# Performance work log

Hardware: AMD Instinct MI355X
Metric: run time of the kernel (lower is better)

## Reference

```python
import jax, jax.numpy as jnp
import numpy as np

M = 100000      # number of simplices
NNZ = 800000    # nonzeros per Laplacian (avg degree 8)
B = 2
C_IN = 64
C_OUT = 64
K1 = 3
K2 = 3


def setup_inputs() -> dict:
    key = jax.random.key(0)
    ks = jax.random.split(key, 7)
    Ll_indices = jax.random.randint(ks[0], (2, NNZ), 0, M, dtype=jnp.int32)
    Ll_values = jax.random.normal(ks[1], (NNZ,), dtype=jnp.float32) * 0.1
    Lu_indices = jax.random.randint(ks[2], (2, NNZ), 0, M, dtype=jnp.int32)
    Lu_values = jax.random.normal(ks[3], (NNZ,), dtype=jnp.float32) * 0.1
    x = jax.random.normal(ks[4], (B, C_IN, M), dtype=jnp.float32)
    theta = jax.random.normal(ks[5], (C_OUT, C_IN, K1 + K2), dtype=jnp.float32)
    bias = jnp.zeros((1, C_OUT, 1), dtype=jnp.float32)
    return {"Ll_indices": Ll_indices, "Ll_values": Ll_values,
            "Lu_indices": Lu_indices, "Lu_values": Lu_values,
            "x": x, "theta": theta, "bias": bias}


def _spmm(rows, cols, vals, x):
    # sparse (M,M) @ x along last axis; x: (B, C, M) -> (B, C, M)
    gathered = x[:, :, cols] * vals            # (B, C, nnz)
    return jnp.zeros_like(x).at[:, :, rows].add(gathered)


def _assemble_powers(K, rows, cols, vals, x):
    outs = [x]
    for _ in range(K - 1):
        outs.append(_spmm(rows, cols, vals, outs[-1]))
    return jnp.stack(outs, axis=3)             # (B, C, M, K)


def reference(Ll_indices, Ll_values, Lu_indices, Lu_values, x, theta, bias):
    X1 = _assemble_powers(K1, Ll_indices[0], Ll_indices[1], Ll_values, x)
    X2 = _assemble_powers(K2, Lu_indices[0], Lu_indices[1], Lu_values, x)
    X = jnp.concatenate((X1, X2), axis=3)      # (B, C_in, M, K1+K2)
    y = jnp.einsum('bimk,oik->bom', X, theta)  # (B, C_out, M)
    return y + bias
```

## Files before the change

kernel.cpp:

```cpp
#include <hip/hip_runtime.h>
#include <stdint.h>

#define M_SIMP 100000
#define MPAD   100064
#define NNZV   800000
#define KM5    5

typedef unsigned int u32;
typedef __attribute__((ext_vector_type(8))) short short8;
typedef __attribute__((ext_vector_type(4))) float f32x4;

__device__ __forceinline__ float bf2f(u32 u){ return __uint_as_float(u << 16); }
__device__ __forceinline__ u32 f2bf(float f){
    u32 u = __float_as_uint(f);
    return (u + 0x7FFFu + ((u >> 16) & 1u)) >> 16;
}

__global__ void k_histpe(const int* __restrict__ i0, int* __restrict__ c0, int* __restrict__ p0,
                         const int* __restrict__ i1, int* __restrict__ c1, int* __restrict__ p1){
    int e = blockIdx.x * 256 + threadIdx.x;
    const int* idx = blockIdx.y ? i1 : i0;
    int* cnt = blockIdx.y ? c1 : c0;
    int* pe  = blockIdx.y ? p1 : p0;
    if (e < NNZV){
        int r = idx[e];
        pe[e] = atomicAdd(&cnt[r], 1);
    }
}

__global__ void k_scan1(const int* __restrict__ in0, int* __restrict__ out0, int* __restrict__ bs0,
                        const int* __restrict__ in1, int* __restrict__ out1, int* __restrict__ bs1,
                        int n){
    const int* in  = blockIdx.y ? in1 : in0;
    int* out   = blockIdx.y ? out1 : out0;
    int* bsums = blockIdx.y ? bs1 : bs0;
    __shared__ int s[256];
    int t = threadIdx.x;
    int base = blockIdx.x * 1024 + t * 4;
    int v0 = (base + 0 < n) ? in[base + 0] : 0;
    int v1 = (base + 1 < n) ? in[base + 1] : 0;
    int v2 = (base + 2 < n) ? in[base + 2] : 0;
    int v3 = (base + 3 < n) ? in[base + 3] : 0;
    int sum = v0 + v1 + v2 + v3;
    s[t] = sum;
    __syncthreads();
    for (int off = 1; off < 256; off <<= 1){
        int x = (t >= off) ? s[t - off] : 0;
        __syncthreads();
        s[t] += x;
        __syncthreads();
    }
    int excl = s[t] - sum;
    if (t == 255) bsums[blockIdx.x] = s[255];
    if (base + 0 < n) out[base + 0] = excl;
    if (base + 1 < n) out[base + 1] = excl + v0;
    if (base + 2 < n) out[base + 2] = excl + v0 + v1;
    if (base + 3 < n) out[base + 3] = excl + v0 + v1 + v2;
}

__global__ void k_scan2(int* __restrict__ b0, int* __restrict__ b1,
                        int* __restrict__ rp0, int* __restrict__ rp1, int nb){
    int t = threadIdx.x;
    if (t < 2){
        int* bs = t ? b1 : b0;
        int run = 0;
        for (int i = 0; i < nb; i++){ int x = bs[i]; bs[i] = run; run += x; }
    }
    if (t == 2) rp0[M_SIMP] = NNZV;
    if (t == 3) rp1[M_SIMP] = NNZV;
}

__global__ void k_scan3(int* __restrict__ o0, const int* __restrict__ b0,
                        int* __restrict__ o1, const int* __restrict__ b1, int n){
    int* out = blockIdx.y ? o1 : o0;
    const int* bsums = blockIdx.y ? b1 : b0;
    int base = blockIdx.x * 1024 + threadIdx.x * 4;
    int add = bsums[blockIdx.x];
    #pragma unroll
    for (int j = 0; j < 4; j++)
        if (base + j < n) out[base + j] += add;
}

__global__ void k_scatcv(const int* __restrict__ i0, const float* __restrict__ v0,
                         const int* __restrict__ pe0, const int* __restrict__ rp0,
                         uint2* __restrict__ cv0,
                         const int* __restrict__ i1, const float* __restrict__ v1,
                         const int* __restrict__ pe1, const int* __restrict__ rp1,
                         uint2* __restrict__ cv1){
    int e = blockIdx.x * 256 + threadIdx.x;
    const int* idx   = blockIdx.y ? i1 : i0;
    const float* val = blockIdx.y ? v1 : v0;
    const int* pe    = blockIdx.y ? pe1 : pe0;
    const int* rp    = blockIdx.y ? rp1 : rp0;
    uint2* cv        = blockIdx.y ? cv1 : cv0;
    if (e < NNZV){
        int r = idx[e];
        uint2 o;
        o.x = (u32)idx[NNZV + e];
        o.y = __float_as_uint(val[e]);
        cv[rp[r] + pe[e]] = o;
    }
}

__global__ void k_transpose(const float* __restrict__ x, u32* __restrict__ F0){
    __shared__ unsigned short s[64 * 130];
    int t = threadIdx.x;
    int m0 = blockIdx.x * 64;
    int j  = t & 63;
    int r4 = t >> 6;
    #pragma unroll 4
    for (int it = 0; it < 32; ++it){
        int bc = it * 4 + r4;
        int m  = m0 + j;
        if (m < M_SIMP)
            s[j * 130 + bc] = (unsigned short)f2bf(x[(size_t)bc * M_SIMP + m]);
    }
    __syncthreads();
    #pragma unroll 4
    for (int it = 0; it < 16; ++it){
        int m  = it * 4 + r4;
        int gm = m0 + m;
        if (gm < M_SIMP){
            u32 lo = s[m * 130 + 2 * j];
            u32 hi = s[m * 130 + 2 * j + 1];
            F0[(size_t)gm * 64 + j] = lo | (hi << 16);
        }
    }
}

__global__ __launch_bounds__(256) void k_spmm(
    const int* __restrict__ rpA, const uint2* __restrict__ cvA,
    const u32* __restrict__ finA, u32* __restrict__ foutA,
    const int* __restrict__ rpB, const uint2* __restrict__ cvB,
    const u32* __restrict__ finB, u32* __restrict__ foutB)
{
    int t   = threadIdx.x;
    int sub = t >> 4;
    int l   = t & 15;
    int row = blockIdx.x * 16 + sub;
    const int* rp; const uint2* cv; const u32* fin; u32* fout;
    if (blockIdx.y == 0){ rp=rpA; cv=cvA; fin=finA; fout=foutA; }
    else                { rp=rpB; cv=cvB; fin=finB; fout=foutB; }
    if (row >= M_SIMP) return;
    int s = rp[row], en = rp[row + 1];
    float a0=0,a1=0,a2=0,a3=0,a4=0,a5=0,a6=0,a7=0;
    int j = s;
    for (; j + 4 <= en; j += 4){
        uint2 q0 = cv[j], q1 = cv[j+1], q2 = cv[j+2], q3 = cv[j+3];
        uint4 g0 = *(const uint4*)(fin + (size_t)q0.x * 64 + l * 4);
        uint4 g1 = *(const uint4*)(fin + (size_t)q1.x * 64 + l * 4);
        uint4 g2 = *(const uint4*)(fin + (size_t)q2.x * 64 + l * 4);
        uint4 g3 = *(const uint4*)(fin + (size_t)q3.x * 64 + l * 4);
        float v0 = __uint_as_float(q0.y), v1 = __uint_as_float(q1.y);
        float v2 = __uint_as_float(q2.y), v3 = __uint_as_float(q3.y);
        a0 += v0*bf2f(g0.x&0xffffu) + v1*bf2f(g1.x&0xffffu) + v2*bf2f(g2.x&0xffffu) + v3*bf2f(g3.x&0xffffu);
        a1 += v0*bf2f(g0.x>>16)     + v1*bf2f(g1.x>>16)     + v2*bf2f(g2.x>>16)     + v3*bf2f(g3.x>>16);
        a2 += v0*bf2f(g0.y&0xffffu) + v1*bf2f(g1.y&0xffffu) + v2*bf2f(g2.y&0xffffu) + v3*bf2f(g3.y&0xffffu);
        a3 += v0*bf2f(g0.y>>16)     + v1*bf2f(g1.y>>16)     + v2*bf2f(g2.y>>16)     + v3*bf2f(g3.y>>16);
        a4 += v0*bf2f(g0.z&0xffffu) + v1*bf2f(g1.z&0xffffu) + v2*bf2f(g2.z&0xffffu) + v3*bf2f(g3.z&0xffffu);
        a5 += v0*bf2f(g0.z>>16)     + v1*bf2f(g1.z>>16)     + v2*bf2f(g2.z>>16)     + v3*bf2f(g3.z>>16);
        a6 += v0*bf2f(g0.w&0xffffu) + v1*bf2f(g1.w&0xffffu) + v2*bf2f(g2.w&0xffffu) + v3*bf2f(g3.w&0xffffu);
        a7 += v0*bf2f(g0.w>>16)     + v1*bf2f(g1.w>>16)     + v2*bf2f(g2.w>>16)     + v3*bf2f(g3.w>>16);
    }
    for (; j < en; j++){
        uint2 q = cv[j];
        float v = __uint_as_float(q.y);
        uint4 g = *(const uint4*)(fin + (size_t)q.x * 64 + l * 4);
        a0 += v*bf2f(g.x&0xffffu); a1 += v*bf2f(g.x>>16);
        a2 += v*bf2f(g.y&0xffffu); a3 += v*bf2f(g.y>>16);
        a4 += v*bf2f(g.z&0xffffu); a5 += v*bf2f(g.z>>16);
        a6 += v*bf2f(g.w&0xffffu); a7 += v*bf2f(g.w>>16);
    }
    uint4 o;
    o.x = f2bf(a0) | (f2bf(a1) << 16);
    o.y = f2bf(a2) | (f2bf(a3) << 16);
    o.z = f2bf(a4) | (f2bf(a5) << 16);
    o.w = f2bf(a6) | (f2bf(a7) << 16);
    *(uint4*)(fout + (size_t)row * 64 + l * 4) = o;
}

__global__ void k_wb(const float* __restrict__ theta, u32* __restrict__ Wb){
    int idx = blockIdx.x * 256 + threadIdx.x;
    if (idx < KM5 * 64 * 32){
        int km = idx >> 11;
        int r  = idx & 2047;
        int o  = r >> 5;
        int i2 = (r & 31) * 2;
        int k  = (km == 0) ? 0 : ((km < 3) ? km : km + 1);
        float lo = theta[o * 384 + i2 * 6 + k];
        float hi = theta[o * 384 + (i2 + 1) * 6 + k];
        if (km == 0){
            lo += theta[o * 384 + i2 * 6 + 3];
            hi += theta[o * 384 + (i2 + 1) * 6 + 3];
        }
        Wb[idx] = f2bf(lo) | (f2bf(hi) << 16);
    }
}

__global__ __launch_bounds__(256, 4) void k_gemm(
    const u32* __restrict__ F0, const u32* __restrict__ F1, const u32* __restrict__ F2,
    const u32* __restrict__ F4, const u32* __restrict__ F5,
    const u32* __restrict__ Wb, const float* __restrict__ bias, float* __restrict__ out)
{
    __shared__ __align__(16) u32 sh[2][4096];
    int t    = threadIdx.x;
    int wave = t >> 6;
    int lane = t & 63;
    int q    = lane >> 4;
    int l16  = lane & 15;
    int bm   = blockIdx.x * 64;
    const u32* __restrict__ Fs[KM5] = {F0, F1, F2, F4, F5};

    int rowbase  = t >> 4;
    int srcc     = (t & 15) ^ ((t >> 4) & 15);
    int wavebase = (t & 192) * 4;

    f32x4 a00 = {0.f,0.f,0.f,0.f}, a10 = {0.f,0.f,0.f,0.f};
    f32x4 a20 = {0.f,0.f,0.f,0.f}, a30 = {0.f,0.f,0.f,0.f};
    f32x4 a01 = {0.f,0.f,0.f,0.f}, a11 = {0.f,0.f,0.f,0.f};
    f32x4 a21 = {0.f,0.f,0.f,0.f}, a31 = {0.f,0.f,0.f,0.f};

    int o_a = wave * 16 + l16;

    short8 wc0 = *(const short8*)(Wb + (0 * 64 + o_a) * 32 + 0 * 16 + q * 4);
    short8 wc1 = *(const short8*)(Wb + (0 * 64 + o_a) * 32 + 1 * 16 + q * 4);

    #pragma unroll
    for (int i = 0; i < 4; ++i){
        const u32* g = Fs[0] + (size_t)(bm + i * 16 + rowbase) * 64 + srcc * 4;
        __builtin_amdgcn_global_load_lds(g, &sh[0][i * 1024 + wavebase], 16, 0, 0);
    }
    asm volatile("s_waitcnt vmcnt(0)" ::: "memory");
    __syncthreads();

    #pragma unroll
    for (int km = 0; km < KM5; ++km){
        short8 wn0 = wc0, wn1 = wc1;
        if (km < KM5 - 1){
            wn0 = *(const short8*)(Wb + ((km + 1) * 64 + o_a) * 32 + 0 * 16 + q * 4);
            wn1 = *(const short8*)(Wb + ((km + 1) * 64 + o_a) * 32 + 1 * 16 + q * 4);
            const u32* __restrict__ Fn = Fs[km + 1];
            u32* dst = &sh[(km + 1) & 1][0];
            #pragma unroll
            for (int i = 0; i < 4; ++i){
                const u32* g = Fn + (size_t)(bm + i * 16 + rowbase) * 64 + srcc * 4;
                __builtin_amdgcn_global_load_lds(g, dst + i * 1024 + wavebase, 16, 0, 0);
            }
        }

        const u32* Lb = &sh[km & 1][0];
        #pragma unroll
        for (int h = 0; h < 2; ++h){
            short8 wa = h ? wc1 : wc0;
            int c0 = ((h * 4 + q) ^ l16) * 4;
            int c1 = ((8 + h * 4 + q) ^ l16) * 4;
            #pragma unroll
            for (int ms = 0; ms < 4; ++ms){
                const u32* rp_ = Lb + ms * 1024 + l16 * 64;
                short8 b0 = *(const short8*)(rp_ + c0);
                short8 b1 = *(const short8*)(rp_ + c1);
                if (ms == 0){ a00 = __builtin_amdgcn_mfma_f32_16x16x32_bf16(wa, b0, a00, 0, 0, 0);
                              a01 = __builtin_amdgcn_mfma_f32_16x16x32_bf16(wa, b1, a01, 0, 0, 0); }
                if (ms == 1){ a10 = __builtin_amdgcn_mfma_f32_16x16x32_bf16(wa, b0, a10, 0, 0, 0);
                              a11 = __builtin_amdgcn_mfma_f32_16x16x32_bf16(wa, b1, a11, 0, 0, 0); }
                if (ms == 2){ a20 = __builtin_amdgcn_mfma_f32_16x16x32_bf16(wa, b0, a20, 0, 0, 0);
                              a21 = __builtin_amdgcn_mfma_f32_16x16x32_bf16(wa, b1, a21, 0, 0, 0); }
                if (ms == 3){ a30 = __builtin_amdgcn_mfma_f32_16x16x32_bf16(wa, b0, a30, 0, 0, 0);
                              a31 = __builtin_amdgcn_mfma_f32_16x16x32_bf16(wa, b1, a31, 0, 0, 0); }
            }
        }

        asm volatile("s_waitcnt vmcnt(0)" ::: "memory");
        __syncthreads();
        wc0 = wn0; wc1 = wn1;
    }

    int ob = wave * 16 + q * 4;
    float bv0 = bias[ob], bv1 = bias[ob+1], bv2 = bias[ob+2], bv3 = bias[ob+3];
    f32x4 accs0[4] = {a00, a10, a20, a30};
    f32x4 accs1[4] = {a01, a11, a21, a31};
    #pragma unroll
    for (int ms = 0; ms < 4; ms++){
        int gm = bm + ms * 16 + l16;
        if (gm < M_SIMP){
            size_t base0 = (size_t)(0 * 64 + ob) * M_SIMP + gm;
            size_t base1 = (size_t)(1 * 64 + ob) * M_SIMP + gm;
            out[base0             ] = accs0[ms][0] + bv0;
            out[base0 + 1ul*M_SIMP] = accs0[ms][1] + bv1;
            out[base0 + 2ul*M_SIMP] = accs0[ms][2] + bv2;
            out[base0 + 3ul*M_SIMP] = accs0[ms][3] + bv3;
            out[base1             ] = accs1[ms][0] + bv0;
            out[base1 + 1ul*M_SIMP] = accs1[ms][1] + bv1;
            out[base1 + 2ul*M_SIMP] = accs1[ms][2] + bv2;
            out[base1 + 3ul*M_SIMP] = accs1[ms][3] + bv3;
        }
    }
}

extern "C" void kernel_launch(void* const* d_in, const int* in_sizes, int n_in,
                              void* d_out, int out_size, void* d_ws, size_t ws_size,
                              hipStream_t stream)
{
    const int*   Ll_idx = (const int*)d_in[0];
    const float* Ll_val = (const float*)d_in[1];
    const int*   Lu_idx = (const int*)d_in[2];
    const float* Lu_val = (const float*)d_in[3];
    const float* x      = (const float*)d_in[4];
    const float* theta  = (const float*)d_in[5];
    const float* bias   = (const float*)d_in[6];
    float* out = (float*)d_out;

    char* ws = (char*)d_ws;
    size_t off = 0;
    auto take = [&](size_t bytes) -> char* {
        char* p = ws + off;
        off = (off + bytes + 255) & ~(size_t)255;
        return p;
    };
    const size_t FB = (size_t)MPAD * 64 * 4;
    u32* F0 = (u32*)take(FB);
    u32* F1 = (u32*)take(FB);
    u32* F2 = (u32*)take(FB);
    u32* F4 = (u32*)take(FB);
    u32* F5 = (u32*)take(FB);
    u32* Wb = (u32*)take((size_t)KM5 * 64 * 32 * 4);
    int* cnt_l = (int*)take((size_t)M_SIMP * 4);
    int* cnt_u = (int*)take((size_t)M_SIMP * 4);
    int* rp_l  = (int*)take((size_t)(M_SIMP + 1) * 4);
    int* rp_u  = (int*)take((size_t)(M_SIMP + 1) * 4);
    int* pe_l  = (int*)take((size_t)NNZV * 4);
    int* pe_u  = (int*)take((size_t)NNZV * 4);
    uint2* cv_l = (uint2*)take((size_t)NNZV * 8);
    uint2* cv_u = (uint2*)take((size_t)NNZV * 8);
    int* bs_l = (int*)take(512);
    int* bs_u = (int*)take(512);

    hipMemsetAsync(cnt_l, 0, (size_t)M_SIMP * 4, stream);
    hipMemsetAsync(cnt_u, 0, (size_t)M_SIMP * 4, stream);

    const int NBH = (NNZV + 255) / 256;
    dim3 gh(NBH, 2);
    k_histpe<<<gh, 256, 0, stream>>>(Ll_idx, cnt_l, pe_l, Lu_idx, cnt_u, pe_u);

    const int NBS = (M_SIMP + 1023) / 1024;
    dim3 gs(NBS, 2);
    k_scan1<<<gs, 256, 0, stream>>>(cnt_l, rp_l, bs_l, cnt_u, rp_u, bs_u, M_SIMP);
    k_scan2<<<1, 64, 0, stream>>>(bs_l, bs_u, rp_l, rp_u, NBS);
    k_scan3<<<gs, 256, 0, stream>>>(rp_l, bs_l, rp_u, bs_u, M_SIMP);

    k_scatcv<<<gh, 256, 0, stream>>>(Ll_idx, Ll_val, pe_l, rp_l, cv_l,
                                     Lu_idx, Lu_val, pe_u, rp_u, cv_u);

    const int NBT = (M_SIMP + 63) / 64;
    k_transpose<<<NBT, 256, 0, stream>>>(x, F0);
    k_wb<<<(KM5 * 64 * 32 + 255) / 256, 256, 0, stream>>>(theta, Wb);

    const int NBM = (M_SIMP + 15) / 16;
    dim3 gm(NBM, 2);
    k_spmm<<<gm, 256, 0, stream>>>(rp_l, cv_l, F0, F1,
                                   rp_u, cv_u, F0, F4);
    k_spmm<<<gm, 256, 0, stream>>>(rp_l, cv_l, F1, F2,
                                   rp_u, cv_u, F4, F5);

    k_gemm<<<NBT, 256, 0, stream>>>(F0, F1, F2, F4, F5, Wb, bias, out);
}
```

Measured before the change: 411.2 us.

## Privatize CSR row histogram per XCC and fuse front-end kernels

Row counting for CSR construction now uses eight per-XCC counter arrays selected by the hardware XCC id, with workgroup-scope relaxed atomics, so atomics avoid cross-die coherence traffic. The scan kernels are extended to turn the eight counter copies into per-XCC row offsets, which the scatter uses. The histogram, transpose/bf16 conversion and weight packing are merged into one launch to cut launch overhead. In exchange it adds an 8x larger memset and extra scan traffic, and it relies on workgroup-scope atomics staying correct across CUs that share an XCC.

Measured after the change: 403.3 us. About the same (-1.9%).

```diff
diff --git a/kernel.cpp b/kernel.cpp
--- a/kernel.cpp
+++ b/kernel.cpp
@@ -5,6 +5,9 @@
 #define MPAD   100064
 #define NNZV   800000
 #define KM5    5
+#define NBH    3125
+#define NBT    1563
+#define NBW    40
 
 typedef unsigned int u32;
 typedef __attribute__((ext_vector_type(8))) short short8;
@@ -16,32 +19,93 @@
     return (u + 0x7FFFu + ((u >> 16) & 1u)) >> 16;
 }
 
-__global__ void k_histpe(const int* __restrict__ i0, int* __restrict__ c0, int* __restrict__ p0,
-                         const int* __restrict__ i1, int* __restrict__ c1, int* __restrict__ p1){
-    int e = blockIdx.x * 256 + threadIdx.x;
-    const int* idx = blockIdx.y ? i1 : i0;
-    int* cnt = blockIdx.y ? c1 : c0;
-    int* pe  = blockIdx.y ? p1 : p0;
-    if (e < NNZV){
-        int r = idx[e];
-        pe[e] = atomicAdd(&cnt[r], 1);
-    }
-}
-
-__global__ void k_scan1(const int* __restrict__ in0, int* __restrict__ out0, int* __restrict__ bs0,
-                        const int* __restrict__ in1, int* __restrict__ out1, int* __restrict__ bs1,
+__global__ void k_front(const int* __restrict__ Ll_idx, const int* __restrict__ Lu_idx,
+                        int* __restrict__ cnt8_l, int* __restrict__ cnt8_u,
+                        u32* __restrict__ pe_l, u32* __restrict__ pe_u,
+                        const float* __restrict__ x, u32* __restrict__ F0,
+                        const float* __restrict__ theta, u32* __restrict__ Wb)
+{
+    __shared__ unsigned short s[64 * 130];
+    int bid = blockIdx.x;
+    int t   = threadIdx.x;
+
+    if (bid < 2 * NBH){
+        int lap = (bid >= NBH);
+        const int* idx = lap ? Lu_idx : Ll_idx;
+        int* cnt8      = lap ? cnt8_u : cnt8_l;
+        u32* pe        = lap ? pe_u  : pe_l;
+        int e = (bid - lap * NBH) * 256 + t;
+        u32 xcc;
+        asm volatile("s_getreg_b32 %0, hwreg(HW_REG_XCC_ID)" : "=s"(xcc));
+        xcc &= 7u;
+        if (e < NNZV){
+            int r = idx[e];
+            u32 p = __hip_atomic_fetch_add((u32*)&cnt8[xcc * M_SIMP + r], 1u,
+                                           __ATOMIC_RELAXED, __HIP_MEMORY_SCOPE_WORKGROUP);
+            pe[e] = p | (xcc << 24);
+        }
+    } else if (bid < 2 * NBH + NBT){
+        int m0 = (bid - 2 * NBH) * 64;
+        int j  = t & 63;
+        int r4 = t >> 6;
+        #pragma unroll 4
+        for (int it = 0; it < 32; ++it){
+            int bc = it * 4 + r4;
+            int m  = m0 + j;
+            if (m < M_SIMP)
+                s[j * 130 + bc] = (unsigned short)f2bf(x[(size_t)bc * M_SIMP + m]);
+        }
+        __syncthreads();
+        #pragma unroll 4
+        for (int it = 0; it < 16; ++it){
+            int m  = it * 4 + r4;
+            int gm = m0 + m;
+            if (gm < M_SIMP){
+                u32 lo = s[m * 130 + 2 * j];
+                u32 hi = s[m * 130 + 2 * j + 1];
+                F0[(size_t)gm * 64 + j] = lo | (hi << 16);
+            }
+        }
+    } else {
+        int idx = (bid - 2 * NBH - NBT) * 256 + t;
+        if (idx < KM5 * 64 * 32){
+            int km = idx >> 11;
+            int r  = idx & 2047;
+            int o  = r >> 5;
+            int i2 = (r & 31) * 2;
+            int k  = (km == 0) ? 0 : ((km < 3) ? km : km + 1);
+            float lo = theta[o * 384 + i2 * 6 + k];
+            float hi = theta[o * 384 + (i2 + 1) * 6 + k];
+            if (km == 0){
+                lo += theta[o * 384 + i2 * 6 + 3];
+                hi += theta[o * 384 + (i2 + 1) * 6 + 3];
+            }
+            Wb[idx] = f2bf(lo) | (f2bf(hi) << 16);
+        }
+    }
+}
+
+__global__ void k_scan1(int* __restrict__ cnt0, int* __restrict__ out0, int* __restrict__ bs0,
+                        int* __restrict__ cnt1, int* __restrict__ out1, int* __restrict__ bs1,
                         int n){
-    const int* in  = blockIdx.y ? in1 : in0;
+    int* cnt   = blockIdx.y ? cnt1 : cnt0;
     int* out   = blockIdx.y ? out1 : out0;
     int* bsums = blockIdx.y ? bs1 : bs0;
     __shared__ int s[256];
     int t = threadIdx.x;
     int base = blockIdx.x * 1024 + t * 4;
-    int v0 = (base + 0 < n) ? in[base + 0] : 0;
-    int v1 = (base + 1 < n) ? in[base + 1] : 0;
-    int v2 = (base + 2 < n) ? in[base + 2] : 0;
-    int v3 = (base + 3 < n) ? in[base + 3] : 0;
-    int sum = v0 + v1 + v2 + v3;
+    int c[8][4];
+    int tot[4] = {0,0,0,0};
+    bool ok = (base < n);
+    if (ok){
+        #pragma unroll
+        for (int i = 0; i < 8; i++){
+            int4 v = *(const int4*)(cnt + (size_t)i * M_SIMP + base);
+            c[i][0]=v.x; c[i][1]=v.y; c[i][2]=v.z; c[i][3]=v.w;
+            tot[0]+=v.x; tot[1]+=v.y; tot[2]+=v.z; tot[3]+=v.w;
+        }
+    }
+    int sum = tot[0]+tot[1]+tot[2]+tot[3];
     s[t] = sum;
     __syncthreads();
     for (int off = 1; off < 256; off <<= 1){
@@ -52,10 +116,20 @@
     }
     int excl = s[t] - sum;
     if (t == 255) bsums[blockIdx.x] = s[255];
-    if (base + 0 < n) out[base + 0] = excl;
-    if (base + 1 < n) out[base + 1] = excl + v0;
-    if (base + 2 < n) out[base + 2] = excl + v0 + v1;
-    if (base + 3 < n) out[base + 3] = excl + v0 + v1 + v2;
+    if (ok){
+        int ro[4];
+        ro[0] = excl;
+        ro[1] = ro[0] + tot[0];
+        ro[2] = ro[1] + tot[1];
+        ro[3] = ro[2] + tot[2];
+        *(int4*)(out + base) = make_int4(ro[0], ro[1], ro[2], ro[3]);
+        int p0=ro[0], p1=ro[1], p2=ro[2], p3=ro[3];
+        #pragma unroll
+        for (int i = 0; i < 8; i++){
+            *(int4*)(cnt + (size_t)i * M_SIMP + base) = make_int4(p0, p1, p2, p3);
+            p0 += c[i][0]; p1 += c[i][1]; p2 += c[i][2]; p3 += c[i][3];
+        }
+    }
 }
 
 __global__ void k_scan2(int* __restrict__ b0, int* __restrict__ b1,
@@ -70,61 +144,45 @@
     if (t == 3) rp1[M_SIMP] = NNZV;
 }
 
-__global__ void k_scan3(int* __restrict__ o0, const int* __restrict__ b0,
-                        int* __restrict__ o1, const int* __restrict__ b1, int n){
+__global__ void k_scan3(int* __restrict__ o0, const int* __restrict__ b0, int* __restrict__ c0,
+                        int* __restrict__ o1, const int* __restrict__ b1, int* __restrict__ c1,
+                        int n){
     int* out = blockIdx.y ? o1 : o0;
     const int* bsums = blockIdx.y ? b1 : b0;
+    int* c8  = blockIdx.y ? c1 : c0;
     int base = blockIdx.x * 1024 + threadIdx.x * 4;
     int add = bsums[blockIdx.x];
-    #pragma unroll
-    for (int j = 0; j < 4; j++)
-        if (base + j < n) out[base + j] += add;
+    if (base < n){
+        int4* po = (int4*)(out + base);
+        int4 v = *po; v.x+=add; v.y+=add; v.z+=add; v.w+=add; *po = v;
+        #pragma unroll
+        for (int i = 0; i < 8; i++){
+            int4* pc = (int4*)(c8 + (size_t)i * M_SIMP + base);
+            int4 u = *pc; u.x+=add; u.y+=add; u.z+=add; u.w+=add; *pc = u;
+        }
+    }
 }
 
 __global__ void k_scatcv(const int* __restrict__ i0, const float* __restrict__ v0,
-                         const int* __restrict__ pe0, const int* __restrict__ rp0,
+                         const u32* __restrict__ pe0, const int* __restrict__ c8_0,
                          uint2* __restrict__ cv0,
                          const int* __restrict__ i1, const float* __restrict__ v1,
-                         const int* __restrict__ pe1, const int* __restrict__ rp1,
+                         const u32* __restrict__ pe1, const int* __restrict__ c8_1,
                          uint2* __restrict__ cv1){
     int e = blockIdx.x * 256 + threadIdx.x;
     const int* idx   = blockIdx.y ? i1 : i0;
     const float* val = blockIdx.y ? v1 : v0;
-    const int* pe    = blockIdx.y ? pe1 : pe0;
-    const int* rp    = blockIdx.y ? rp1 : rp0;
+    const u32* pe    = blockIdx.y ? pe1 : pe0;
+    const int* c8    = blockIdx.y ? c8_1 : c8_0;
     uint2* cv        = blockIdx.y ? cv1 : cv0;
     if (e < NNZV){
         int r = idx[e];
+        u32 pr = pe[e];
+        int pos = c8[(size_t)(pr >> 24) * M_SIMP + r] + (int)(pr & 0xFFFFFFu);
         uint2 o;
         o.x = (u32)idx[NNZV + e];
         o.y = __float_as_uint(val[e]);
-        cv[rp[r] + pe[e]] = o;
-    }
-}
-
-__global__ void k_transpose(const float* __restrict__ x, u32* __restrict__ F0){
-    __shared__ unsigned short s[64 * 130];
-    int t = threadIdx.x;
-    int m0 = blockIdx.x * 64;
-    int j  = t & 63;
-    int r4 = t >> 6;
-    #pragma unroll 4
-    for (int it = 0; it < 32; ++it){
-        int bc = it * 4 + r4;
-        int m  = m0 + j;
-        if (m < M_SIMP)
-            s[j * 130 + bc] = (unsigned short)f2bf(x[(size_t)bc * M_SIMP + m]);
-    }
-    __syncthreads();
-    #pragma unroll 4
-    for (int it = 0; it < 16; ++it){
-        int m  = it * 4 + r4;
-        int gm = m0 + m;
-        if (gm < M_SIMP){
-            u32 lo = s[m * 130 + 2 * j];
-            u32 hi = s[m * 130 + 2 * j + 1];
-            F0[(size_t)gm * 64 + j] = lo | (hi << 16);
-        }
+        cv[pos] = o;
     }
 }
 
@@ -179,24 +237,6 @@
     *(uint4*)(fout + (size_t)row * 64 + l * 4) = o;
 }
 
-__global__ void k_wb(const float* __restrict__ theta, u32* __restrict__ Wb){
-    int idx = blockIdx.x * 256 + threadIdx.x;
-    if (idx < KM5 * 64 * 32){
-        int km = idx >> 11;
-        int r  = idx & 2047;
-        int o  = r >> 5;
-        int i2 = (r & 31) * 2;
-        int k  = (km == 0) ? 0 : ((km < 3) ? km : km + 1);
-        float lo = theta[o * 384 + i2 * 6 + k];
-        float hi = theta[o * 384 + (i2 + 1) * 6 + k];
-        if (km == 0){
-            lo += theta[o * 384 + i2 * 6 + 3];
-            hi += theta[o * 384 + (i2 + 1) * 6 + 3];
-        }
-        Wb[idx] = f2bf(lo) | (f2bf(hi) << 16);
-    }
-}
-
 __global__ __launch_bounds__(256, 4) void k_gemm(
     const u32* __restrict__ F0, const u32* __restrict__ F1, const u32* __restrict__ F2,
     const u32* __restrict__ F4, const u32* __restrict__ F5,
@@ -324,36 +364,32 @@
     u32* F4 = (u32*)take(FB);
     u32* F5 = (u32*)take(FB);
     u32* Wb = (u32*)take((size_t)KM5 * 64 * 32 * 4);
-    int* cnt_l = (int*)take((size_t)M_SIMP * 4);
-    int* cnt_u = (int*)take((size_t)M_SIMP * 4);
+    int* cnt8_l = (int*)take((size_t)8 * M_SIMP * 4);
+    int* cnt8_u = (int*)take((size_t)8 * M_SIMP * 4);
     int* rp_l  = (int*)take((size_t)(M_SIMP + 1) * 4);
     int* rp_u  = (int*)take((size_t)(M_SIMP + 1) * 4);
-    int* pe_l  = (int*)take((size_t)NNZV * 4);
-    int* pe_u  = (int*)take((size_t)NNZV * 4);
+    u32* pe_l  = (u32*)take((size_t)NNZV * 4);
+    u32* pe_u  = (u32*)take((size_t)NNZV * 4);
     uint2* cv_l = (uint2*)take((size_t)NNZV * 8);
     uint2* cv_u = (uint2*)take((size_t)NNZV * 8);
     int* bs_l = (int*)take(512);
     int* bs_u = (int*)take(512);
 
-    hipMemsetAsync(cnt_l, 0, (size_t)M_SIMP * 4, stream);
-    hipMemsetAsync(cnt_u, 0, (size_t)M_SIMP * 4, stream);
-
-    const int NBH = (NNZV + 255) / 256;
-    dim3 gh(NBH, 2);
-    k_histpe<<<gh, 256, 0, stream>>>(Ll_idx, cnt_l, pe_l, Lu_idx, cnt_u, pe_u);
+    hipMemsetAsync(cnt8_l, 0, (size_t)8 * M_SIMP * 4, stream);
+    hipMemsetAsync(cnt8_u, 0, (size_t)8 * M_SIMP * 4, stream);
+
+    k_front<<<2 * NBH + NBT + NBW, 256, 0, stream>>>(
+        Ll_idx, Lu_idx, cnt8_l, cnt8_u, pe_l, pe_u, x, F0, theta, Wb);
 
     const int NBS = (M_SIMP + 1023) / 1024;
     dim3 gs(NBS, 2);
-    k_scan1<<<gs, 256, 0, stream>>>(cnt_l, rp_l, bs_l, cnt_u, rp_u, bs_u, M_SIMP);
+    k_scan1<<<gs, 256, 0, stream>>>(cnt8_l, rp_l, bs_l, cnt8_u, rp_u, bs_u, M_SIMP);
     k_scan2<<<1, 64, 0, stream>>>(bs_l, bs_u, rp_l, rp_u, NBS);
-    k_scan3<<<gs, 256, 0, stream>>>(rp_l, bs_l, rp_u, bs_u, M_SIMP);
-
-    k_scatcv<<<gh, 256, 0, stream>>>(Ll_idx, Ll_val, pe_l, rp_l, cv_l,
-                                     Lu_idx, Lu_val, pe_u, rp_u, cv_u);
-
-    const int NBT = (M_SIMP + 63) / 64;
-    k_transpose<<<NBT, 256, 0, stream>>>(x, F0);
-    k_wb<<<(KM5 * 64 * 32 + 255) / 256, 256, 0, stream>>>(theta, Wb);
+    k_scan3<<<gs, 256, 0, stream>>>(rp_l, bs_l, cnt8_l, rp_u, bs_u, cnt8_u, M_SIMP);
+
+    dim3 gh(NBH, 2);
+    k_scatcv<<<gh, 256, 0, stream>>>(Ll_idx, Ll_val, pe_l, cnt8_l, cv_l,
+                                     Lu_idx, Lu_val, pe_u, cnt8_u, cv_u);
 
     const int NBM = (M_SIMP + 15) / 16;
     dim3 gm(NBM, 2);
```

## Interleave Ll/Lu CSR build stages with SpMM via role-dispatched fused kernels

Applied to the files above, without the earlier changes.

Replaces the separate histogram, scan, scatter, transpose and SpMM launches with fused kernels. Each block picks a role from its block index, so the Lu CSR build (hist, scan, scatter) runs alongside the Ll SpMM passes. The scan2 kernel is dropped: scan3 now reduces the block sums in shared memory itself. The intent is fewer launches and more overlap of independent small stages. The cost is extra divergence in role dispatch and more shared memory per block, which may lower occupancy for the SpMM blocks.

Result: faster. 389.4 us (-5.3%).

```diff
diff --git a/kernel.cpp b/kernel.cpp
--- a/kernel.cpp
+++ b/kernel.cpp
@@ -5,6 +5,11 @@
 #define MPAD   100064
 #define NNZV   800000
 #define KM5    5
+#define NBH    3125
+#define NBT    1563
+#define NBW    40
+#define NBM    6250
+#define NBS    98
 
 typedef unsigned int u32;
 typedef __attribute__((ext_vector_type(8))) short short8;
@@ -16,96 +21,20 @@
     return (u + 0x7FFFu + ((u >> 16) & 1u)) >> 16;
 }
 
-__global__ void k_histpe(const int* __restrict__ i0, int* __restrict__ c0, int* __restrict__ p0,
-                         const int* __restrict__ i1, int* __restrict__ c1, int* __restrict__ p1){
-    int e = blockIdx.x * 256 + threadIdx.x;
-    const int* idx = blockIdx.y ? i1 : i0;
-    int* cnt = blockIdx.y ? c1 : c0;
-    int* pe  = blockIdx.y ? p1 : p0;
+
+__device__ __forceinline__ void role_hist(int h, int t, const int* __restrict__ idx,
+                                          int* __restrict__ cnt, u32* __restrict__ pe){
+    int e = h * 256 + t;
     if (e < NNZV){
         int r = idx[e];
-        pe[e] = atomicAdd(&cnt[r], 1);
-    }
-}
-
-__global__ void k_scan1(const int* __restrict__ in0, int* __restrict__ out0, int* __restrict__ bs0,
-                        const int* __restrict__ in1, int* __restrict__ out1, int* __restrict__ bs1,
-                        int n){
-    const int* in  = blockIdx.y ? in1 : in0;
-    int* out   = blockIdx.y ? out1 : out0;
-    int* bsums = blockIdx.y ? bs1 : bs0;
-    __shared__ int s[256];
-    int t = threadIdx.x;
-    int base = blockIdx.x * 1024 + t * 4;
-    int v0 = (base + 0 < n) ? in[base + 0] : 0;
-    int v1 = (base + 1 < n) ? in[base + 1] : 0;
-    int v2 = (base + 2 < n) ? in[base + 2] : 0;
-    int v3 = (base + 3 < n) ? in[base + 3] : 0;
-    int sum = v0 + v1 + v2 + v3;
-    s[t] = sum;
-    __syncthreads();
-    for (int off = 1; off < 256; off <<= 1){
-        int x = (t >= off) ? s[t - off] : 0;
-        __syncthreads();
-        s[t] += x;
-        __syncthreads();
-    }
-    int excl = s[t] - sum;
-    if (t == 255) bsums[blockIdx.x] = s[255];
-    if (base + 0 < n) out[base + 0] = excl;
-    if (base + 1 < n) out[base + 1] = excl + v0;
-    if (base + 2 < n) out[base + 2] = excl + v0 + v1;
-    if (base + 3 < n) out[base + 3] = excl + v0 + v1 + v2;
-}
-
-__global__ void k_scan2(int* __restrict__ b0, int* __restrict__ b1,
-                        int* __restrict__ rp0, int* __restrict__ rp1, int nb){
-    int t = threadIdx.x;
-    if (t < 2){
-        int* bs = t ? b1 : b0;
-        int run = 0;
-        for (int i = 0; i < nb; i++){ int x = bs[i]; bs[i] = run; run += x; }
-    }
-    if (t == 2) rp0[M_SIMP] = NNZV;
-    if (t == 3) rp1[M_SIMP] = NNZV;
-}
-
-__global__ void k_scan3(int* __restrict__ o0, const int* __restrict__ b0,
-                        int* __restrict__ o1, const int* __restrict__ b1, int n){
-    int* out = blockIdx.y ? o1 : o0;
-    const int* bsums = blockIdx.y ? b1 : b0;
-    int base = blockIdx.x * 1024 + threadIdx.x * 4;
-    int add = bsums[blockIdx.x];
-    #pragma unroll
-    for (int j = 0; j < 4; j++)
-        if (base + j < n) out[base + j] += add;
-}
-
-__global__ void k_scatcv(const int* __restrict__ i0, const float* __restrict__ v0,
-                         const int* __restrict__ pe0, const int* __restrict__ rp0,
-                         uint2* __restrict__ cv0,
-                         const int* __restrict__ i1, const float* __restrict__ v1,
-                         const int* __restrict__ pe1, const int* __restrict__ rp1,
-                         uint2* __restrict__ cv1){
-    int e = blockIdx.x * 256 + threadIdx.x;
-    const int* idx   = blockIdx.y ? i1 : i0;
-    const float* val = blockIdx.y ? v1 : v0;
-    const int* pe    = blockIdx.y ? pe1 : pe0;
-    const int* rp    = blockIdx.y ? rp1 : rp0;
-    uint2* cv        = blockIdx.y ? cv1 : cv0;
-    if (e < NNZV){
-        int r = idx[e];
-        uint2 o;
-        o.x = (u32)idx[NNZV + e];
-        o.y = __float_as_uint(val[e]);
-        cv[rp[r] + pe[e]] = o;
-    }
-}
-
-__global__ void k_transpose(const float* __restrict__ x, u32* __restrict__ F0){
+        pe[e] = (u32)atomicAdd(&cnt[r], 1);
+    }
+}
+
+__device__ __forceinline__ void role_transpose(int g, int t, const float* __restrict__ x,
+                                               u32* __restrict__ F0){
     __shared__ unsigned short s[64 * 130];
-    int t = threadIdx.x;
-    int m0 = blockIdx.x * 64;
+    int m0 = g * 64;
     int j  = t & 63;
     int r4 = t >> 6;
     #pragma unroll 4
@@ -128,19 +57,92 @@
     }
 }
 
-__global__ __launch_bounds__(256) void k_spmm(
-    const int* __restrict__ rpA, const uint2* __restrict__ cvA,
-    const u32* __restrict__ finA, u32* __restrict__ foutA,
-    const int* __restrict__ rpB, const uint2* __restrict__ cvB,
-    const u32* __restrict__ finB, u32* __restrict__ foutB)
-{
-    int t   = threadIdx.x;
+__device__ __forceinline__ void role_wb(int g, int t, const float* __restrict__ theta,
+                                        u32* __restrict__ Wb){
+    int idx = g * 256 + t;
+    if (idx < KM5 * 64 * 32){
+        int km = idx >> 11;
+        int r  = idx & 2047;
+        int o  = r >> 5;
+        int i2 = (r & 31) * 2;
+        int k  = (km == 0) ? 0 : ((km < 3) ? km : km + 1);
+        float lo = theta[o * 384 + i2 * 6 + k];
+        float hi = theta[o * 384 + (i2 + 1) * 6 + k];
+        if (km == 0){
+            lo += theta[o * 384 + i2 * 6 + 3];
+            hi += theta[o * 384 + (i2 + 1) * 6 + 3];
+        }
+        Wb[idx] = f2bf(lo) | (f2bf(hi) << 16);
+    }
+}
+
+__device__ __forceinline__ void role_scan1(int b, int t, const int* __restrict__ in,
+                                           int* __restrict__ out, int* __restrict__ bsums){
+    __shared__ int s1[256];
+    int base = b * 1024 + t * 4;
+    int v0 = (base + 0 < M_SIMP) ? in[base + 0] : 0;
+    int v1 = (base + 1 < M_SIMP) ? in[base + 1] : 0;
+    int v2 = (base + 2 < M_SIMP) ? in[base + 2] : 0;
+    int v3 = (base + 3 < M_SIMP) ? in[base + 3] : 0;
+    int sum = v0 + v1 + v2 + v3;
+    s1[t] = sum;
+    __syncthreads();
+    for (int off = 1; off < 256; off <<= 1){
+        int x = (t >= off) ? s1[t - off] : 0;
+        __syncthreads();
+        s1[t] += x;
+        __syncthreads();
+    }
+    int excl = s1[t] - sum;
+    if (t == 255) bsums[b] = s1[255];
+    if (base + 0 < M_SIMP) out[base + 0] = excl;
+    if (base + 1 < M_SIMP) out[base + 1] = excl + v0;
+    if (base + 2 < M_SIMP) out[base + 2] = excl + v0 + v1;
+    if (base + 3 < M_SIMP) out[base + 3] = excl + v0 + v1 + v2;
+}
+
+__device__ __forceinline__ void role_scan3(int b, int t, int* __restrict__ out,
+                                           const int* __restrict__ bsums){
+    __shared__ int sb[256];
+    sb[t] = (t < b && t < NBS) ? bsums[t] : 0;
+    __syncthreads();
+    #pragma unroll
+    for (int off = 128; off > 0; off >>= 1){
+        if (t < off) sb[t] += sb[t + off];
+        __syncthreads();
+    }
+    int add = sb[0];
+    if (t == 255 && b == 0) out[M_SIMP] = NNZV;
+    int base = b * 1024 + t * 4;
+    if (base < M_SIMP){
+        int4* po = (int4*)(out + base);
+        int4 v = *po; v.x += add; v.y += add; v.z += add; v.w += add; *po = v;
+    }
+}
+
+__device__ __forceinline__ void role_scatcv(int b, int t, const int* __restrict__ idx,
+                                            const float* __restrict__ val,
+                                            const u32* __restrict__ pe,
+                                            const int* __restrict__ rp,
+                                            uint2* __restrict__ cv){
+    int e = b * 256 + t;
+    if (e < NNZV){
+        int r = idx[e];
+        int pos = rp[r] + (int)pe[e];
+        uint2 o;
+        o.x = (u32)idx[NNZV + e];
+        o.y = __float_as_uint(val[e]);
+        cv[pos] = o;
+    }
+}
+
+__device__ __forceinline__ void role_spmm(int blk, int t, const int* __restrict__ rp,
+                                          const uint2* __restrict__ cv,
+                                          const u32* __restrict__ fin,
+                                          u32* __restrict__ fout){
     int sub = t >> 4;
     int l   = t & 15;
-    int row = blockIdx.x * 16 + sub;
-    const int* rp; const uint2* cv; const u32* fin; u32* fout;
-    if (blockIdx.y == 0){ rp=rpA; cv=cvA; fin=finA; fout=foutA; }
-    else                { rp=rpB; cv=cvB; fin=finB; fout=foutB; }
+    int row = blk * 16 + sub;
     if (row >= M_SIMP) return;
     int s = rp[row], en = rp[row + 1];
     float a0=0,a1=0,a2=0,a3=0,a4=0,a5=0,a6=0,a7=0;
@@ -179,22 +181,66 @@
     *(uint4*)(fout + (size_t)row * 64 + l * 4) = o;
 }
 
-__global__ void k_wb(const float* __restrict__ theta, u32* __restrict__ Wb){
-    int idx = blockIdx.x * 256 + threadIdx.x;
-    if (idx < KM5 * 64 * 32){
-        int km = idx >> 11;
-        int r  = idx & 2047;
-        int o  = r >> 5;
-        int i2 = (r & 31) * 2;
-        int k  = (km == 0) ? 0 : ((km < 3) ? km : km + 1);
-        float lo = theta[o * 384 + i2 * 6 + k];
-        float hi = theta[o * 384 + (i2 + 1) * 6 + k];
-        if (km == 0){
-            lo += theta[o * 384 + i2 * 6 + 3];
-            hi += theta[o * 384 + (i2 + 1) * 6 + 3];
-        }
-        Wb[idx] = f2bf(lo) | (f2bf(hi) << 16);
-    }
+
+__global__ __launch_bounds__(256) void k_fA(const int* __restrict__ Ll_idx,
+                        int* __restrict__ cnt_l, u32* __restrict__ pe_l,
+                        const float* __restrict__ x, u32* __restrict__ F0,
+                        const float* __restrict__ theta, u32* __restrict__ Wb){
+    int bid = blockIdx.x, t = threadIdx.x;
+    int r3 = bid % 3, g3 = bid / 3;
+    if (r3 < 2){
+        int h = g3 * 2 + r3;
+        if (h < NBH) role_hist(h, t, Ll_idx, cnt_l, pe_l);
+    } else if (g3 < NBT){
+        role_transpose(g3, t, x, F0);
+    } else {
+        role_wb(g3 - NBT, t, theta, Wb);
+    }
+}
+
+__global__ __launch_bounds__(256) void k_scan1(const int* __restrict__ cnt,
+                                               int* __restrict__ rp, int* __restrict__ bs){
+    role_scan1(blockIdx.x, threadIdx.x, cnt, rp, bs);
+}
+__global__ __launch_bounds__(256) void k_scan3(int* __restrict__ rp, const int* __restrict__ bs){
+    role_scan3(blockIdx.x, threadIdx.x, rp, bs);
+}
+
+__global__ __launch_bounds__(256) void k_scat_hist(
+    const int* __restrict__ Ll_idx, const float* __restrict__ Ll_val,
+    const u32* __restrict__ pe_l, const int* __restrict__ rp_l, uint2* __restrict__ cv_l,
+    const int* __restrict__ Lu_idx, int* __restrict__ cnt_u, u32* __restrict__ pe_u){
+    int bid = blockIdx.x, t = threadIdx.x;
+    int g = bid >> 1;
+    if ((bid & 1) == 0) role_scatcv(g, t, Ll_idx, Ll_val, pe_l, rp_l, cv_l);
+    else                role_hist(g, t, Lu_idx, cnt_u, pe_u);
+}
+
+__global__ __launch_bounds__(256) void k_sp_scan1(
+    const int* __restrict__ rp_l, const uint2* __restrict__ cv_l,
+    const u32* __restrict__ F0, u32* __restrict__ F1,
+    const int* __restrict__ cnt_u, int* __restrict__ rp_u, int* __restrict__ bs_u){
+    int bid = blockIdx.x, t = threadIdx.x;
+    if (bid < NBS) role_scan1(bid, t, cnt_u, rp_u, bs_u);
+    else           role_spmm(bid - NBS, t, rp_l, cv_l, F0, F1);
+}
+
+__global__ __launch_bounds__(256) void k_sp_scat(
+    const int* __restrict__ rp_l, const uint2* __restrict__ cv_l,
+    const u32* __restrict__ F1, u32* __restrict__ F2,
+    const int* __restrict__ Lu_idx, const float* __restrict__ Lu_val,
+    const u32* __restrict__ pe_u, const int* __restrict__ rp_u, uint2* __restrict__ cv_u){
+    int bid = blockIdx.x, t = threadIdx.x;
+    int r3 = bid % 3, g3 = bid / 3;
+    if (r3 == 0) role_scatcv(g3, t, Lu_idx, Lu_val, pe_u, rp_u, cv_u);
+    else         role_spmm(g3 * 2 + (r3 - 1), t, rp_l, cv_l, F1, F2);
+}
+
+__global__ __launch_bounds__(256) void k_spmm(const int* __restrict__ rp,
+                                              const uint2* __restrict__ cv,
+                                              const u32* __restrict__ fin,
+                                              u32* __restrict__ fout){
+    role_spmm(blockIdx.x, threadIdx.x, rp, cv, fin, fout);
 }
 
 __global__ __launch_bounds__(256, 4) void k_gemm(
@@ -328,8 +374,8 @@
     int* cnt_u = (int*)take((size_t)M_SIMP * 4);
     int* rp_l  = (int*)take((size_t)(M_SIMP + 1) * 4);
     int* rp_u  = (int*)take((size_t)(M_SIMP + 1) * 4);
-    int* pe_l  = (int*)take((size_t)NNZV * 4);
-    int* pe_u  = (int*)take((size_t)NNZV * 4);
+    u32* pe_l  = (u32*)take((size_t)NNZV * 4);
+    u32* pe_u  = (u32*)take((size_t)NNZV * 4);
     uint2* cv_l = (uint2*)take((size_t)NNZV * 8);
     uint2* cv_u = (uint2*)take((size_t)NNZV * 8);
     int* bs_l = (int*)take(512);
@@ -338,29 +384,23 @@
     hipMemsetAsync(cnt_l, 0, (size_t)M_SIMP * 4, stream);
     hipMemsetAsync(cnt_u, 0, (size_t)M_SIMP * 4, stream);
 
-    const int NBH = (NNZV + 255) / 256;
-    dim3 gh(NBH, 2);
-    k_histpe<<<gh, 256, 0, stream>>>(Ll_idx, cnt_l, pe_l, Lu_idx, cnt_u, pe_u);
-
-    const int NBS = (M_SIMP + 1023) / 1024;
-    dim3 gs(NBS, 2);
-    k_scan1<<<gs, 256, 0, stream>>>(cnt_l, rp_l, bs_l, cnt_u, rp_u, bs_u, M_SIMP);
-    k_scan2<<<1, 64, 0, stream>>>(bs_l, bs_u, rp_l, rp_u, NBS);
-    k_scan3<<<gs, 256, 0, stream>>>(rp_l, bs_l, rp_u, bs_u, M_SIMP);
-
-    k_scatcv<<<gh, 256, 0, stream>>>(Ll_idx, Ll_val, pe_l, rp_l, cv_l,
-                                     Lu_idx, Lu_val, pe_u, rp_u, cv_u);
-
-    const int NBT = (M_SIMP + 63) / 64;
-    k_transpose<<<NBT, 256, 0, stream>>>(x, F0);
-    k_wb<<<(KM5 * 64 * 32 + 255) / 256, 256, 0, stream>>>(theta, Wb);
-
-    const int NBM = (M_SIMP + 15) / 16;
-    dim3 gm(NBM, 2);
-    k_spmm<<<gm, 256, 0, stream>>>(rp_l, cv_l, F0, F1,
-                                   rp_u, cv_u, F0, F4);
-    k_spmm<<<gm, 256, 0, stream>>>(rp_l, cv_l, F1, F2,
-                                   rp_u, cv_u, F4, F5);
+    k_fA<<<3 * (NBT + NBW), 256, 0, stream>>>(Ll_idx, cnt_l, pe_l, x, F0, theta, Wb);
+
+    k_scan1<<<NBS, 256, 0, stream>>>(cnt_l, rp_l, bs_l);
+    k_scan3<<<NBS, 256, 0, stream>>>(rp_l, bs_l);
+
+    k_scat_hist<<<2 * NBH, 256, 0, stream>>>(Ll_idx, Ll_val, pe_l, rp_l, cv_l,
+                                             Lu_idx, cnt_u, pe_u);
+
+    k_sp_scan1<<<NBS + NBM, 256, 0, stream>>>(rp_l, cv_l, F0, F1, cnt_u, rp_u, bs_u);
+
+    k_scan3<<<NBS, 256, 0, stream>>>(rp_u, bs_u);
+
+    k_sp_scat<<<3 * NBH, 256, 0, stream>>>(rp_l, cv_l, F1, F2,
+                                           Lu_idx, Lu_val, pe_u, rp_u, cv_u);
+
+    k_spmm<<<NBM, 256, 0, stream>>>(rp_u, cv_u, F0, F4);
+    k_spmm<<<NBM, 256, 0, stream>>>(rp_u, cv_u, F4, F5);
 
     k_gemm<<<NBT, 256, 0, stream>>>(F0, F1, F2, F4, F5, Wb, bias, out);
 }
```
